# Kernel tuning notes

Hardware: AMD Instinct MI355X
Metric: run time of the kernel (lower is better)

## Reference

```python
import jax, jax.numpy as jnp
import numpy as np

M_POW = 4   # m: number of visual-graph powers
N_POW = 4   # n: number of text-graph powers
T = 32      # temporal length, forced by torch.eye(32) in GraphFusion
EPS_BN = 1e-5


def conv1d_same(x, w, b):
    # x: (B, Cin, L), w: (Cout, Cin, 3) -> (B, Cout, L), padding=1
    y = jax.lax.conv_general_dilated(x, w, window_strides=(1,), padding=[(1, 1)],
                                     dimension_numbers=("NCH", "OIH", "NCH"))
    return y + b[None, :, None]


def setup_inputs() -> dict:
    key = jax.random.key(0)
    ks = jax.random.split(key, 10)
    b, c = 128, 5
    d = {}
    d["v_feature"] = jax.random.normal(ks[0], (b, c, T, 2048), jnp.float32)
    d["t_feature"] = jax.random.normal(ks[1], (b, c, T, 768), jnp.float32)
    # Temporal embedding convs (Conv1d k=3, pad=1)
    d["wv"] = jax.random.normal(ks[2], (32, 2048, 3), jnp.float32) * 0.02
    d["bv"] = jnp.zeros((32,), jnp.float32)
    d["wt"] = jax.random.normal(ks[3], (32, 768, 3), jnp.float32) * 0.02
    d["bt"] = jnp.zeros((32,), jnp.float32)
    # GraphFusion learned (m, n) bilinear matrix: torch.normal(0, 1)
    d["fusion_a"] = jax.random.normal(ks[4], (M_POW, N_POW), jnp.float32)
    # NormalHead (BN-WVAD style, in_channel=32, hidden 2 -> 1 -> 1, all k=1 convs)
    d["w1"] = jax.random.normal(ks[5], (2, 32), jnp.float32) * 0.1
    d["b1"] = jnp.zeros((2,), jnp.float32)
    d["g1"] = jnp.ones((2,), jnp.float32)
    d["be1"] = jnp.zeros((2,), jnp.float32)
    d["w2"] = jax.random.normal(ks[6], (1, 2), jnp.float32) * 0.1
    d["b2"] = jnp.zeros((1,), jnp.float32)
    d["g2"] = jnp.ones((1,), jnp.float32)
    d["be2"] = jnp.zeros((1,), jnp.float32)
    d["w3"] = jax.random.normal(ks[7], (1, 1), jnp.float32) * 0.1
    d["b3"] = jnp.zeros((1,), jnp.float32)
    return d


def _forward(v_feature, t_feature, wv, bv, wt, bt, fusion_a,
             w1, b1, g1, be1, w2, b2, g2, be2, w3, b3):
    b, c, t, feat_v = v_feature.shape
    B = b * c
    fv = v_feature.reshape(B, t, feat_v)
    ft = t_feature.reshape(B, t, t_feature.shape[3])
    # Temporal: permute -> conv1d(k=3,pad=1) -> relu -> permute
    fv = jax.nn.relu(conv1d_same(fv.transpose(0, 2, 1), wv, bv)).transpose(0, 2, 1)  # (B,t,32)
    ft = jax.nn.relu(conv1d_same(ft.transpose(0, 2, 1), wt, bt)).transpose(0, 2, 1)  # (B,t,32)

    # GraphFusion
    def l2n(x):
        return x / jnp.maximum(jnp.linalg.norm(x, axis=2, keepdims=True), 1e-12)
    f_v = l2n(fv)
    f_t = l2n(ft)
    a_v = jax.nn.relu(jnp.einsum('bid,bjd->bij', f_v, f_v))  # (B,t,t)
    a_t = jax.nn.relu(jnp.einsum('bid,bjd->bij', f_t, f_t))  # (B,t,t)
    eye = jnp.broadcast_to(jnp.eye(t, dtype=a_v.dtype), (B, t, t))
    # power 0 replaced by identity, as in the torch code
    av_p = jnp.stack([eye] + [a_v ** i for i in range(1, M_POW)], axis=0)  # (m,B,t,t)
    at_p = jnp.stack([eye] + [a_t ** j for j in range(1, N_POW)], axis=0)  # (n,B,t,t)
    # einsum('bijk,kl,blij->bij') with the permutes undone == 'kbij,kl,lbij->bij'
    a_fused = jnp.einsum('kbij,kl,lbij->bij', av_p, fusion_a, at_p)
    a_fused = jax.nn.relu(a_fused)
    a_fused = a_fused / (jnp.max(a_fused) + 0.01)

    # NormalHead on x = a_fused.permute(0,2,1) : (B, C=t, L=t)
    x = a_fused.transpose(0, 2, 1)

    def bn(h, g, beta):  # training-mode BatchNorm1d over (N, L) per channel
        mu = h.mean(axis=(0, 2), keepdims=True)
        var = h.var(axis=(0, 2), keepdims=True)
        return (h - mu) * jax.lax.rsqrt(var + EPS_BN) * g[None, :, None] + beta[None, :, None]

    x1 = jnp.einsum('oc,bcl->bol', w1, x) + b1[None, :, None]
    h1 = jax.nn.relu(bn(x1, g1, be1))
    x2 = jnp.einsum('oc,bcl->bol', w2, h1) + b2[None, :, None]
    h2 = jax.nn.relu(bn(x2, g2, be2))
    scores = jax.nn.sigmoid(jnp.einsum('oc,bcl->bol', w3, h2) + b3[None, :, None])  # (B,1,t)
    normal_scores = scores.reshape(b, c, t).mean(axis=1)  # (b, t), crop-averaged
    return (normal_scores, a_v, a_t, a_fused)


def reference(v_feature, t_feature, wv, bv, wt, bt, fusion_a,
              w1, b1, g1, be1, w2, b2, g2, be2, w3, b3):
    return _forward(v_feature, t_feature, wv, bv, wt, bt, fusion_a,
                    w1, b1, g1, be1, w2, b2, g2, be2, w3, b3)
```

## Files before the change

kernel.cpp:

```cpp
#include <hip/hip_runtime.h>
#include <hip/hip_bf16.h>
#include <math.h>


typedef __attribute__((ext_vector_type(8))) short short8;
typedef __attribute__((ext_vector_type(4))) float f32x4;

#define XROW 136

__device__ __forceinline__ unsigned short f2bf(float f) {
    __hip_bfloat16 h = __float2bfloat16(f);
    return *reinterpret_cast<unsigned short*>(&h);
}
__device__ __forceinline__ float bf2f(unsigned short u) {
    return __uint_as_float(((unsigned int)u) << 16);
}
__device__ __forceinline__ short8 lds_frag(const unsigned short* p) {
    union { uint4 u; short8 s; } r;
    r.u = *reinterpret_cast<const uint4*>(p);
    return r.s;
}
__device__ __forceinline__ short8 glb_frag(const unsigned short* p) {
    union { uint4 u; short8 s; } r;
    r.u = *reinterpret_cast<const uint4*>(p);
    return r.s;
}

__global__ __launch_bounds__(256) void pack_kernel(
    const float* __restrict__ wv, const float* __restrict__ wt,
    unsigned short* __restrict__ wvpk, unsigned short* __restrict__ wtpk,
    float* __restrict__ scal, float* __restrict__ fv, float* __restrict__ ft) {
    int gid = blockIdx.x * 256 + threadIdx.x;
    if (gid < 16) scal[gid] = 0.f;
    for (int i = gid; i < 655360; i += 270336) {
        fv[i] = 0.f;
        ft[i] = 0.f;
    }
    const int NV = 196608, NT = 73728;
    if (gid < NV) {
        int o = gid / 6144, rem = gid % 6144;
        int c = rem / 3, k = rem % 3;
        int s = c >> 5, cp = c & 31;
        int tn = o >> 4, m = o & 15, quad = cp >> 3, j = cp & 7;
        float f = wv[gid];
        unsigned short h = f2bf(f);
        unsigned short l = f2bf(f - bf2f(h));
        int base = (s * 3 + k) * 2048 + tn * 1024 + ((quad << 4) + m) * 8 + j;
        wvpk[base] = h;
        wvpk[base + 512] = l;
    } else if (gid < NV + NT) {
        int g = gid - NV;
        int o = g / 2304, rem = g % 2304;
        int c = rem / 3, k = rem % 3;
        int s = c >> 5, cp = c & 31;
        int tn = o >> 4, m = o & 15, quad = cp >> 3, j = cp & 7;
        float f = wt[g];
        unsigned short h = f2bf(f);
        unsigned short l = f2bf(f - bf2f(h));
        int base = (s * 3 + k) * 2048 + tn * 1024 + ((quad << 4) + m) * 8 + j;
        wtpk[base] = h;
        wtpk[base + 512] = l;
    }
}

__device__ __forceinline__ void conv_phase(
    const float* __restrict__ xb, int Cin,
    const unsigned short* __restrict__ wpk,
    unsigned short* hiT, unsigned short* loT,
    float* __restrict__ yout, int tid, int wave, int lane, int part) {
    int tm = wave & 1, tn = wave >> 1;
    int m = lane & 15, quad = lane >> 4;
    int c4 = tid & 31, tg = tid >> 5;
    int nchunk = Cin >> 7;
    int ch0 = (nchunk * part) >> 2;
    int ch1 = (nchunk * (part + 1)) >> 2;

    const float* xbase = xb + (c4 << 2);
    float4 xq0, xq1, xq2, xq3;
    {
        const float* p = xbase + (size_t)(ch0 << 7);
        xq0 = *reinterpret_cast<const float4*>(p + (size_t)tg * Cin);
        xq1 = *reinterpret_cast<const float4*>(p + (size_t)(tg + 8) * Cin);
        xq2 = *reinterpret_cast<const float4*>(p + (size_t)(tg + 16) * Cin);
        xq3 = *reinterpret_cast<const float4*>(p + (size_t)(tg + 24) * Cin);
    }
    __syncthreads();
    if (tid < XROW) {
        hiT[tid] = 0; hiT[33 * XROW + tid] = 0;
        loT[tid] = 0; loT[33 * XROW + tid] = 0;
    }
    f32x4 acc0 = {0.f, 0.f, 0.f, 0.f};
    f32x4 acc1 = {0.f, 0.f, 0.f, 0.f};

    auto stage = [&](const float4& xq, int t) {
        unsigned short h0 = f2bf(xq.x), h1 = f2bf(xq.y);
        unsigned short h2 = f2bf(xq.z), h3 = f2bf(xq.w);
        unsigned short l0 = f2bf(xq.x - bf2f(h0));
        unsigned short l1 = f2bf(xq.y - bf2f(h1));
        unsigned short l2 = f2bf(xq.z - bf2f(h2));
        unsigned short l3 = f2bf(xq.w - bf2f(h3));
        int widx = (t + 1) * XROW + (c4 << 2);
        *reinterpret_cast<uint2*>(hiT + widx) =
            make_uint2(h0 | ((unsigned int)h1 << 16), h2 | ((unsigned int)h3 << 16));
        *reinterpret_cast<uint2*>(loT + widx) =
            make_uint2(l0 | ((unsigned int)l1 << 16), l2 | ((unsigned int)l3 << 16));
    };

    for (int ch = ch0; ch < ch1; ++ch) {
        __syncthreads();
        stage(xq0, tg);
        stage(xq1, tg + 8);
        stage(xq2, tg + 16);
        stage(xq3, tg + 24);
        __syncthreads();
        if (ch + 1 < ch1) {
            const float* p = xbase + (size_t)((ch + 1) << 7);
            xq0 = *reinterpret_cast<const float4*>(p + (size_t)tg * Cin);
            xq1 = *reinterpret_cast<const float4*>(p + (size_t)(tg + 8) * Cin);
            xq2 = *reinterpret_cast<const float4*>(p + (size_t)(tg + 16) * Cin);
            xq3 = *reinterpret_cast<const float4*>(p + (size_t)(tg + 24) * Cin);
        }
        int sbase = ch << 2;
        int arow0 = (tm << 4) + m;
        int bofs = (tn << 10) + (lane << 3);
#pragma unroll
        for (int sl = 0; sl < 4; ++sl) {
            int acol = (sl << 5) + (quad << 3);
            const unsigned short* bbase = wpk + (size_t)(sbase + sl) * 6144 + bofs;
#pragma unroll
            for (int k = 0; k < 3; ++k) {
                short8 Ah = lds_frag(hiT + (arow0 + k) * XROW + acol);
                short8 Al = lds_frag(loT + (arow0 + k) * XROW + acol);
                short8 Bh = glb_frag(bbase + (k << 11));
                short8 Bl = glb_frag(bbase + (k << 11) + 512);
                acc0 = __builtin_amdgcn_mfma_f32_16x16x32_bf16(Ah, Bh, acc0, 0, 0, 0);
                acc1 = __builtin_amdgcn_mfma_f32_16x16x32_bf16(Ah, Bl, acc1, 0, 0, 0);
                acc1 = __builtin_amdgcn_mfma_f32_16x16x32_bf16(Al, Bh, acc1, 0, 0, 0);
            }
        }
    }
    int ocol = (tn << 4) + m;
#pragma unroll
    for (int r = 0; r < 4; ++r) {
        int t = (tm << 4) + (quad << 2) + r;
        atomicAdd(&yout[t * 32 + ocol], acc0[r] + acc1[r]);
    }
}

__global__ __launch_bounds__(256, 4) void conv_mfma_kernel(
    const float* __restrict__ xv, const unsigned short* __restrict__ wvpk,
    const float* __restrict__ xt, const unsigned short* __restrict__ wtpk,
    float* __restrict__ yv, float* __restrict__ yt) {
    __shared__ unsigned short hiT[34 * XROW], loT[34 * XROW];
    int bx = blockIdx.x;
    int b = bx >> 2, part = bx & 3;
    int tid = threadIdx.x;
    int wave = tid >> 6, lane = tid & 63;
    conv_phase(xv + (size_t)b * 32 * 2048, 2048, wvpk, hiT, loT,
               yv + (size_t)b * 1024, tid, wave, lane, part);
    conv_phase(xt + (size_t)b * 32 * 768, 768, wtpk, hiT, loT,
               yt + (size_t)b * 1024, tid, wave, lane, part);
}

__global__ __launch_bounds__(256) void s2_kernel(
    const float* __restrict__ fvp, const float* __restrict__ ftp,
    const float* __restrict__ bv, const float* __restrict__ bt,
    const float* __restrict__ fuse, float* __restrict__ out_av,
    float* __restrict__ out_at, float* __restrict__ out_af,
    unsigned int* __restrict__ maxslot) {
    int b = blockIdx.x, tid = threadIdx.x;
    __shared__ float Fv[32][33], Ft[32][33], inv[64], wmax[4];
#pragma unroll
    for (int e = 0; e < 4; ++e) {
        int idx = tid + 256 * e;
        int i = idx >> 5, j = idx & 31;
        Fv[i][j] = fmaxf(fvp[b * 1024 + idx] + bv[j], 0.f);
        Ft[i][j] = fmaxf(ftp[b * 1024 + idx] + bt[j], 0.f);
    }
    __syncthreads();
    {
        int row = tid >> 3, cg = (tid & 7) * 4;
        float sv = 0.f, st = 0.f;
#pragma unroll
        for (int q = 0; q < 4; ++q) {
            float v = Fv[row][cg + q]; sv = fmaf(v, v, sv);
            float u = Ft[row][cg + q]; st = fmaf(u, u, st);
        }
        sv += __shfl_xor(sv, 1); sv += __shfl_xor(sv, 2); sv += __shfl_xor(sv, 4);
        st += __shfl_xor(st, 1); st += __shfl_xor(st, 2); st += __shfl_xor(st, 4);
        if ((tid & 7) == 0) {
            inv[row]      = rsqrtf(fmaxf(sv, 1e-24f));
            inv[32 + row] = rsqrtf(fmaxf(st, 1e-24f));
        }
    }
    __syncthreads();
    float fa[16];
#pragma unroll
    for (int q = 0; q < 16; ++q) fa[q] = fuse[q];
    float lmax = 0.f;
#pragma unroll
    for (int e = 0; e < 4; ++e) {
        int idx = tid + 256 * e;
        int i = idx >> 5, j = idx & 31;
        float dv = 0.f, dt_ = 0.f;
        for (int c = 0; c < 32; ++c) {
            dv  = fmaf(Fv[i][c], Fv[j][c], dv);
            dt_ = fmaf(Ft[i][c], Ft[j][c], dt_);
        }
        float av = fmaxf(dv  * inv[i] * inv[j], 0.f);
        float at = fmaxf(dt_ * inv[32 + i] * inv[32 + j], 0.f);
        out_av[b * 1024 + idx] = av;
        out_at[b * 1024 + idx] = at;
        float pv0 = (i == j) ? 1.f : 0.f;
        float pv1 = av, pv2 = av * av, pv3 = pv2 * av;
        float pt1 = at, pt2 = at * at, pt3 = pt2 * at;
        float af = 0.f;
        af += (fa[0] * pv0 + fa[4] * pv1 + fa[8]  * pv2 + fa[12] * pv3) * pv0;
        af += (fa[1] * pv0 + fa[5] * pv1 + fa[9]  * pv2 + fa[13] * pv3) * pt1;
        af += (fa[2] * pv0 + fa[6] * pv1 + fa[10] * pv2 + fa[14] * pv3) * pt2;
        af += (fa[3] * pv0 + fa[7] * pv1 + fa[11] * pv2 + fa[15] * pv3) * pt3;
        float r = fmaxf(af, 0.f);
        out_af[b * 1024 + idx] = r;
        lmax = fmaxf(lmax, r);
    }
    for (int off = 1; off < 64; off <<= 1)
        lmax = fmaxf(lmax, __shfl_xor(lmax, off));
    if ((tid & 63) == 0) wmax[tid >> 6] = lmax;
    __syncthreads();
    if (tid == 0) {
        float mx = fmaxf(fmaxf(wmax[0], wmax[1]), fmaxf(wmax[2], wmax[3]));
        atomicMax(maxslot, __float_as_uint(mx));
    }
}

__global__ __launch_bounds__(256) void s3_kernel(
    float* __restrict__ af, const float* __restrict__ w1,
    const float* __restrict__ b1, float* __restrict__ x1,
    float* __restrict__ scal) {
    int b = blockIdx.x, tid = threadIdx.x;
    __shared__ float A[32][33];
    float inv = 1.0f / (__uint_as_float(((const unsigned int*)scal)[0]) + 0.01f);
#pragma unroll
    for (int e = 0; e < 4; ++e) {
        int idx = tid + 256 * e;
        float v = af[b * 1024 + idx] * inv;
        af[b * 1024 + idx] = v;
        A[idx >> 5][idx & 31] = v;
    }
    __syncthreads();
    if (tid < 64) {
        int o = tid >> 5, l = tid & 31;
        float s = b1[o];
        for (int c = 0; c < 32; ++c) s = fmaf(w1[o * 32 + c], A[l][c], s);
        x1[(size_t)(b * 2 + o) * 32 + l] = s;
        float s1 = s, s2 = s * s;
        for (int off = 1; off < 32; off <<= 1) {
            s1 += __shfl_xor(s1, off);
            s2 += __shfl_xor(s2, off);
        }
        if (l == 0) {
            atomicAdd(&scal[1 + o], s1);
            atomicAdd(&scal[3 + o], s2);
        }
    }
}

__global__ __launch_bounds__(256) void s4_kernel(
    const float* __restrict__ x1, const float* __restrict__ g1,
    const float* __restrict__ be1, const float* __restrict__ w2,
    const float* __restrict__ b2, float* __restrict__ x2,
    float* __restrict__ scal) {
    int idx = blockIdx.x * 256 + threadIdx.x;
    const float N = 20480.f;
    float mu0 = scal[1] / N, mu1 = scal[2] / N;
    float va0 = scal[3] / N - mu0 * mu0, va1 = scal[4] / N - mu1 * mu1;
    float rs0 = rsqrtf(va0 + 1e-5f), rs1 = rsqrtf(va1 + 1e-5f);
    int b = idx >> 5, l = idx & 31;
    float h0 = fmaxf((x1[(size_t)(b * 2 + 0) * 32 + l] - mu0) * rs0 * g1[0] + be1[0], 0.f);
    float h1 = fmaxf((x1[(size_t)(b * 2 + 1) * 32 + l] - mu1) * rs1 * g1[1] + be1[1], 0.f);
    float v = w2[0] * h0 + w2[1] * h1 + b2[0];
    x2[idx] = v;
    float s1 = v, s2 = v * v;
    for (int off = 1; off < 64; off <<= 1) {
        s1 += __shfl_xor(s1, off);
        s2 += __shfl_xor(s2, off);
    }
    __shared__ float ps[4][2];
    int lane = threadIdx.x & 63, w = threadIdx.x >> 6;
    if (lane == 0) { ps[w][0] = s1; ps[w][1] = s2; }
    __syncthreads();
    if (threadIdx.x == 0) {
        atomicAdd(&scal[5], ps[0][0] + ps[1][0] + ps[2][0] + ps[3][0]);
        atomicAdd(&scal[6], ps[0][1] + ps[1][1] + ps[2][1] + ps[3][1]);
    }
}

__global__ __launch_bounds__(256) void s5_kernel(
    const float* __restrict__ x2, const float* __restrict__ g2,
    const float* __restrict__ be2, const float* __restrict__ w3,
    const float* __restrict__ b3, float* __restrict__ ns,
    const float* __restrict__ scal) {
    int idx = blockIdx.x * 256 + threadIdx.x;
    const float N = 20480.f;
    float mu = scal[5] / N;
    float var = scal[6] / N - mu * mu;
    float rs = rsqrtf(var + 1e-5f);
    int bb = idx >> 5, t = idx & 31;
    float s = 0.f;
#pragma unroll
    for (int crop = 0; crop < 5; ++crop) {
        int b = bb * 5 + crop;
        float h = fmaxf((x2[b * 32 + t] - mu) * rs * g2[0] + be2[0], 0.f);
        float z = w3[0] * h + b3[0];
        s += 1.f / (1.f + expf(-z));
    }
    ns[idx] = s * 0.2f;
}

extern "C" void kernel_launch(void* const* d_in, const int* in_sizes, int n_in,
                              void* d_out, int out_size, void* d_ws, size_t ws_size,
                              hipStream_t stream) {
    const float* v_feat = (const float*)d_in[0];
    const float* t_feat = (const float*)d_in[1];
    const float* wv  = (const float*)d_in[2];
    const float* bv  = (const float*)d_in[3];
    const float* wt  = (const float*)d_in[4];
    const float* bt  = (const float*)d_in[5];
    const float* fuse= (const float*)d_in[6];
    const float* w1  = (const float*)d_in[7];
    const float* b1  = (const float*)d_in[8];
    const float* g1  = (const float*)d_in[9];
    const float* be1 = (const float*)d_in[10];
    const float* w2  = (const float*)d_in[11];
    const float* b2  = (const float*)d_in[12];
    const float* g2  = (const float*)d_in[13];
    const float* be2 = (const float*)d_in[14];
    const float* w3  = (const float*)d_in[15];
    const float* b3  = (const float*)d_in[16];

    float* ws   = (float*)d_ws;
    float* scal = ws;
    unsigned short* wvpk = (unsigned short*)(ws + 16);
    unsigned short* wtpk = (unsigned short*)(ws + 16 + 196608);
    float* fv   = ws + 16 + 196608 + 73728;
    float* ft   = fv + 655360;
    float* x1   = ft + 655360;
    float* x2   = x1 + 40960;

    float* out_ns = (float*)d_out;
    float* out_av = out_ns + 4096;
    float* out_at = out_av + 655360;
    float* out_af = out_at + 655360;

    pack_kernel<<<1056, 256, 0, stream>>>(wv, wt, wvpk, wtpk, scal, fv, ft);
    conv_mfma_kernel<<<2560, 256, 0, stream>>>(v_feat, wvpk, t_feat, wtpk, fv, ft);
    s2_kernel<<<640, 256, 0, stream>>>(fv, ft, bv, bt, fuse, out_av, out_at,
                                       out_af, (unsigned int*)scal);
    s3_kernel<<<640, 256, 0, stream>>>(out_af, w1, b1, x1, scal);
    s4_kernel<<<80, 256, 0, stream>>>(x1, g1, be1, w2, b2, x2, scal);
    s5_kernel<<<16, 256, 0, stream>>>(x2, g2, be2, w3, b3, out_ns, scal);
}
```

Measured before the change: 380.9 us.

## Fuse first NormalHead conv into s2 using unnormalized fused matrix, rescale BN stats later

Moves the first 1x1 conv (w1) and its BatchNorm statistic accumulation into s2, computing it on the unnormalized fused adjacency held in shared memory. The global-max division is applied afterwards: s4 rescales out_af and folds the scale into the mean and variance algebraically, and the bias b1 cancels under BN. This removes the separate s3 launch and one full read pass over out_af before the max is known. The cost is more work and shared memory in s2, and a change in the floating-point evaluation order of the variance.

```diff
diff --git a/kernel.cpp b/kernel.cpp
--- a/kernel.cpp
+++ b/kernel.cpp
@@ -165,11 +165,12 @@
 __global__ __launch_bounds__(256) void s2_kernel(
     const float* __restrict__ fvp, const float* __restrict__ ftp,
     const float* __restrict__ bv, const float* __restrict__ bt,
-    const float* __restrict__ fuse, float* __restrict__ out_av,
-    float* __restrict__ out_at, float* __restrict__ out_af,
-    unsigned int* __restrict__ maxslot) {
+    const float* __restrict__ fuse, const float* __restrict__ w1,
+    float* __restrict__ out_av, float* __restrict__ out_at,
+    float* __restrict__ out_af, float* __restrict__ u1ws,
+    float* __restrict__ scal) {
     int b = blockIdx.x, tid = threadIdx.x;
-    __shared__ float Fv[32][33], Ft[32][33], inv[64], wmax[4];
+    __shared__ float Fv[32][33], Ft[32][33], Af[32][33], inv[64], wmax[4];
 #pragma unroll
     for (int e = 0; e < 4; ++e) {
         int idx = tid + 256 * e;
@@ -221,6 +222,7 @@
         af += (fa[3] * pv0 + fa[7] * pv1 + fa[11] * pv2 + fa[15] * pv3) * pt3;
         float r = fmaxf(af, 0.f);
         out_af[b * 1024 + idx] = r;
+        Af[i][j] = r;
         lmax = fmaxf(lmax, r);
     }
     for (int off = 1; off < 64; off <<= 1)
@@ -229,30 +231,13 @@
     __syncthreads();
     if (tid == 0) {
         float mx = fmaxf(fmaxf(wmax[0], wmax[1]), fmaxf(wmax[2], wmax[3]));
-        atomicMax(maxslot, __float_as_uint(mx));
-    }
-}
-
-__global__ __launch_bounds__(256) void s3_kernel(
-    float* __restrict__ af, const float* __restrict__ w1,
-    const float* __restrict__ b1, float* __restrict__ x1,
-    float* __restrict__ scal) {
-    int b = blockIdx.x, tid = threadIdx.x;
-    __shared__ float A[32][33];
-    float inv = 1.0f / (__uint_as_float(((const unsigned int*)scal)[0]) + 0.01f);
-#pragma unroll
-    for (int e = 0; e < 4; ++e) {
-        int idx = tid + 256 * e;
-        float v = af[b * 1024 + idx] * inv;
-        af[b * 1024 + idx] = v;
-        A[idx >> 5][idx & 31] = v;
-    }
-    __syncthreads();
+        atomicMax((unsigned int*)scal, __float_as_uint(mx));
+    }
     if (tid < 64) {
         int o = tid >> 5, l = tid & 31;
-        float s = b1[o];
-        for (int c = 0; c < 32; ++c) s = fmaf(w1[o * 32 + c], A[l][c], s);
-        x1[(size_t)(b * 2 + o) * 32 + l] = s;
+        float s = 0.f;
+        for (int c = 0; c < 32; ++c) s = fmaf(w1[o * 32 + c], Af[l][c], s);
+        u1ws[(size_t)(b * 2 + o) * 32 + l] = s;
         float s1 = s, s2 = s * s;
         for (int off = 1; off < 32; off <<= 1) {
             s1 += __shfl_xor(s1, off);
@@ -266,32 +251,37 @@
 }
 
 __global__ __launch_bounds__(256) void s4_kernel(
-    const float* __restrict__ x1, const float* __restrict__ g1,
-    const float* __restrict__ be1, const float* __restrict__ w2,
-    const float* __restrict__ b2, float* __restrict__ x2,
-    float* __restrict__ scal) {
-    int idx = blockIdx.x * 256 + threadIdx.x;
-    const float N = 20480.f;
-    float mu0 = scal[1] / N, mu1 = scal[2] / N;
-    float va0 = scal[3] / N - mu0 * mu0, va1 = scal[4] / N - mu1 * mu1;
-    float rs0 = rsqrtf(va0 + 1e-5f), rs1 = rsqrtf(va1 + 1e-5f);
-    int b = idx >> 5, l = idx & 31;
-    float h0 = fmaxf((x1[(size_t)(b * 2 + 0) * 32 + l] - mu0) * rs0 * g1[0] + be1[0], 0.f);
-    float h1 = fmaxf((x1[(size_t)(b * 2 + 1) * 32 + l] - mu1) * rs1 * g1[1] + be1[1], 0.f);
-    float v = w2[0] * h0 + w2[1] * h1 + b2[0];
-    x2[idx] = v;
-    float s1 = v, s2 = v * v;
-    for (int off = 1; off < 64; off <<= 1) {
-        s1 += __shfl_xor(s1, off);
-        s2 += __shfl_xor(s2, off);
-    }
-    __shared__ float ps[4][2];
-    int lane = threadIdx.x & 63, w = threadIdx.x >> 6;
-    if (lane == 0) { ps[w][0] = s1; ps[w][1] = s2; }
-    __syncthreads();
-    if (threadIdx.x == 0) {
-        atomicAdd(&scal[5], ps[0][0] + ps[1][0] + ps[2][0] + ps[3][0]);
-        atomicAdd(&scal[6], ps[0][1] + ps[1][1] + ps[2][1] + ps[3][1]);
+    float* __restrict__ af, const float* __restrict__ u1,
+    const float* __restrict__ g1, const float* __restrict__ be1,
+    const float* __restrict__ w2, const float* __restrict__ b2,
+    float* __restrict__ x2, const float* __restrict__ scal) {
+    int b = blockIdx.x, tid = threadIdx.x;
+    float invs = 1.0f / (__uint_as_float(((const unsigned int*)scal)[0]) + 0.01f);
+#pragma unroll
+    for (int e = 0; e < 4; ++e) {
+        int idx = tid + 256 * e;
+        af[(size_t)b * 1024 + idx] *= invs;
+    }
+    if (tid < 32) {
+        const float N = 20480.f;
+        float m0 = scal[1] / N, m1 = scal[2] / N;
+        float rs0 = rsqrtf(invs * invs * (scal[3] / N - m0 * m0) + 1e-5f);
+        float rs1 = rsqrtf(invs * invs * (scal[4] / N - m1 * m1) + 1e-5f);
+        float u0 = u1[(size_t)(b * 2 + 0) * 32 + tid];
+        float u1v = u1[(size_t)(b * 2 + 1) * 32 + tid];
+        float h0 = fmaxf(invs * (u0 - m0) * rs0 * g1[0] + be1[0], 0.f);
+        float h1 = fmaxf(invs * (u1v - m1) * rs1 * g1[1] + be1[1], 0.f);
+        float v = w2[0] * h0 + w2[1] * h1 + b2[0];
+        x2[(size_t)b * 32 + tid] = v;
+        float s1 = v, s2 = v * v;
+        for (int off = 1; off < 32; off <<= 1) {
+            s1 += __shfl_xor(s1, off);
+            s2 += __shfl_xor(s2, off);
+        }
+        if (tid == 0) {
+            atomicAdd((float*)&scal[5], s1);
+            atomicAdd((float*)&scal[6], s2);
+        }
     }
 }
 
@@ -337,6 +327,7 @@
     const float* be2 = (const float*)d_in[14];
     const float* w3  = (const float*)d_in[15];
     const float* b3  = (const float*)d_in[16];
+    (void)b1;
 
     float* ws   = (float*)d_ws;
     float* scal = ws;
@@ -344,8 +335,8 @@
     unsigned short* wtpk = (unsigned short*)(ws + 16 + 196608);
     float* fv   = ws + 16 + 196608 + 73728;
     float* ft   = fv + 655360;
-    float* x1   = ft + 655360;
-    float* x2   = x1 + 40960;
+    float* u1   = ft + 655360;
+    float* x2   = u1 + 40960;
 
     float* out_ns = (float*)d_out;
     float* out_av = out_ns + 4096;
@@ -354,9 +345,8 @@
 
     pack_kernel<<<1056, 256, 0, stream>>>(wv, wt, wvpk, wtpk, scal, fv, ft);
     conv_mfma_kernel<<<2560, 256, 0, stream>>>(v_feat, wvpk, t_feat, wtpk, fv, ft);
-    s2_kernel<<<640, 256, 0, stream>>>(fv, ft, bv, bt, fuse, out_av, out_at,
-                                       out_af, (unsigned int*)scal);
-    s3_kernel<<<640, 256, 0, stream>>>(out_af, w1, b1, x1, scal);
-    s4_kernel<<<80, 256, 0, stream>>>(x1, g1, be1, w2, b2, x2, scal);
+    s2_kernel<<<640, 256, 0, stream>>>(fv, ft, bv, bt, fuse, w1, out_av, out_at,
+                                       out_af, u1, scal);
+    s4_kernel<<<640, 256, 0, stream>>>(out_af, u1, g1, be1, w2, b2, x2, scal);
     s5_kernel<<<16, 256, 0, stream>>>(x2, g2, be2, w3, b3, out_ns, scal);
 }
```

Result: slower. 391.5 us (+2.8%).
